# Performance work log

Hardware: AMD Instinct MI355X
Metric: run time of the kernel (lower is better)

## Reference

```python
import jax, jax.numpy as jnp
import numpy as np

B, T, C, HS = 4, 2048, 1024, 64  # batch, seq, n_embd, head_size


def setup_inputs() -> dict:
    key = jax.random.key(0)
    k1, k2, k3, k4 = jax.random.split(key, 4)
    x = jax.random.normal(k1, (B, T, C), dtype=jnp.float32)
    Wq = jax.random.normal(k2, (HS, C), dtype=jnp.float32) * (C ** -0.5)
    Wk = jax.random.normal(k3, (HS, C), dtype=jnp.float32) * (C ** -0.5)
    Wv = jax.random.normal(k4, (HS, C), dtype=jnp.float32) * (C ** -0.5)
    return {"x": x, "Wq": Wq, "Wk": Wk, "Wv": Wv}


def reference(x, Wq, Wk, Wv):
    # q,k,v: [B,T,HS] (nn.Linear: x @ W.T, no bias)
    q = jnp.einsum('btc,hc->bth', x, Wq)
    k = jnp.einsum('btc,hc->bth', x, Wk)
    v = jnp.einsum('btc,hc->bth', x, Wv)
    scale = k.shape[-1] ** -0.5
    wei = jnp.einsum('bth,bsh->bts', q, k) * scale  # [B,T,T]
    # causal mask (tril == 0 -> -inf)
    mask = jnp.tril(jnp.ones((T, T), dtype=bool))
    wei = jnp.where(mask, wei, -jnp.inf)
    wei = jax.nn.softmax(wei, axis=-1)
    # dropout p=0.0 -> identity
    out = jnp.einsum('bts,bsh->bth', wei, v)  # [B,T,HS]
    return out
```

## Files before the change

kernel.cpp:

```cpp
#include <hip/hip_runtime.h>
#include <hip/hip_bf16.h>

#define BB 4
#define TT 2048
#define CC 1024
#define HSZ 64
#define NTOT 8192

typedef __attribute__((ext_vector_type(8))) short bf16x8;
typedef __attribute__((ext_vector_type(4))) float f32x4;

__device__ __forceinline__ unsigned short f2bf(float x) {
    __hip_bfloat16 h = __float2bfloat16(x);
    return *reinterpret_cast<unsigned short*>(&h);
}

__global__ __launch_bounds__(256) void convert_w(
    const float* __restrict__ Wq, const float* __restrict__ Wk,
    const float* __restrict__ Wv, unsigned short* __restrict__ Wh) {
    const int i = blockIdx.x * 256 + threadIdx.x;
    const int c = i >> 8, k4 = (i & 255) * 4;
    float4 wv;
    if (c < 64) {
        wv = *(const float4*)&Wq[(size_t)c * CC + k4];
        wv.x *= 0.125f; wv.y *= 0.125f; wv.z *= 0.125f; wv.w *= 0.125f;
    } else if (c < 128) {
        wv = *(const float4*)&Wk[(size_t)(c - 64) * CC + k4];
    } else {
        wv = *(const float4*)&Wv[(size_t)(c - 128) * CC + k4];
    }
    ushort4 h = {f2bf(wv.x), f2bf(wv.y), f2bf(wv.z), f2bf(wv.w)};
    *(ushort4*)&Wh[(size_t)c * CC + k4] = h;
}

__global__ __launch_bounds__(256) void qkv_mfma(
    const float* __restrict__ x, const unsigned short* __restrict__ Wh,
    unsigned short* __restrict__ qs, unsigned short* __restrict__ ksb,
    unsigned short* __restrict__ vT) {
    __shared__ __align__(16) unsigned short xs[32 * 72];
    __shared__ __align__(16) unsigned short Ws[192 * 72];
    const int tid = threadIdx.x;
    const int w = tid >> 6, lane = tid & 63;
    const int l16 = lane & 15, quad = lane >> 4;
    const int row0 = blockIdx.x * 32;

    const int xrow = tid >> 3, xcol = (tid & 7) * 8;

    float4 xa, xb;
    uint4 wreg0, wreg1, wreg2, wreg3, wreg4, wreg5;

#define LOADX(ch)                                                            \
    {                                                                        \
        const float* p = &x[(size_t)(row0 + xrow) * CC + (ch) * 64 + xcol];  \
        xa = *(const float4*)p;                                              \
        xb = *(const float4*)(p + 4);                                        \
    }
#define LOADW1(it, dst, ch)                                                  \
    {                                                                        \
        const int e = tid + (it) * 256;                                      \
        const int c = e >> 3, g = e & 7;                                     \
        dst = *(const uint4*)&Wh[(size_t)c * CC + (ch) * 64 + g * 8];        \
    }
#define LOADW(ch)                                                            \
    LOADW1(0, wreg0, ch) LOADW1(1, wreg1, ch) LOADW1(2, wreg2, ch)           \
    LOADW1(3, wreg3, ch) LOADW1(4, wreg4, ch) LOADW1(5, wreg5, ch)
#define STOREW1(it, src)                                                     \
    {                                                                        \
        const int e = tid + (it) * 256;                                      \
        const int c = e >> 3, g = e & 7;                                     \
        *(uint4*)&Ws[c * 72 + g * 8] = src;                                  \
    }
#define WRITELDS()                                                           \
    {                                                                        \
        ushort4 h0 = {f2bf(xa.x), f2bf(xa.y), f2bf(xa.z), f2bf(xa.w)};       \
        ushort4 h1 = {f2bf(xb.x), f2bf(xb.y), f2bf(xb.z), f2bf(xb.w)};       \
        *(ushort4*)&xs[xrow * 72 + xcol] = h0;                               \
        *(ushort4*)&xs[xrow * 72 + xcol + 4] = h1;                           \
        STOREW1(0, wreg0) STOREW1(1, wreg1) STOREW1(2, wreg2)                \
        STOREW1(3, wreg3) STOREW1(4, wreg4) STOREW1(5, wreg5)                \
    }

    f32x4 acc[2][3];
#pragma unroll
    for (int m = 0; m < 2; ++m)
#pragma unroll
        for (int n = 0; n < 3; ++n) acc[m][n] = (f32x4){0.f, 0.f, 0.f, 0.f};

    LOADX(0);
    LOADW(0);
    WRITELDS();
    __syncthreads();

    for (int ch = 0; ch < 16; ++ch) {
        if (ch < 15) {
            LOADX(ch + 1);
            LOADW(ch + 1);
        }
        bf16x8 am[2][2], bn[3][2];
#pragma unroll
        for (int m = 0; m < 2; ++m)
#pragma unroll
            for (int h = 0; h < 2; ++h)
                am[m][h] = *(const bf16x8*)&xs[(m * 16 + l16) * 72 + h * 32 + quad * 8];
#pragma unroll
        for (int n = 0; n < 3; ++n)
#pragma unroll
            for (int h = 0; h < 2; ++h)
                bn[n][h] =
                    *(const bf16x8*)&Ws[(w * 48 + n * 16 + l16) * 72 + h * 32 + quad * 8];
#pragma unroll
        for (int h = 0; h < 2; ++h)
#pragma unroll
            for (int m = 0; m < 2; ++m)
#pragma unroll
                for (int n = 0; n < 3; ++n)
                    acc[m][n] = __builtin_amdgcn_mfma_f32_16x16x32_bf16(
                        am[m][h], bn[n][h], acc[m][n], 0, 0, 0);
        if (ch < 15) {
            __syncthreads();
            WRITELDS();
            __syncthreads();
        }
    }

#pragma unroll
    for (int m = 0; m < 2; ++m) {
#pragma unroll
        for (int n = 0; n < 3; ++n) {
            const int col = w * 48 + n * 16 + l16;
            const int r0 = row0 + m * 16 + quad * 4;
            f32x4 a = acc[m][n];
            if (col < 64) {
#pragma unroll
                for (int r = 0; r < 4; ++r)
                    qs[(size_t)(r0 + r) * HSZ + col] = f2bf(a[r]);
            } else if (col < 128) {
#pragma unroll
                for (int r = 0; r < 4; ++r)
                    ksb[(size_t)(r0 + r) * HSZ + (col - 64)] = f2bf(a[r]);
            } else {
                ushort4 pk = {f2bf(a[0]), f2bf(a[1]), f2bf(a[2]), f2bf(a[3])};
                *(ushort4*)&vT[(size_t)(col - 128) * NTOT + r0] = pk;
            }
        }
    }
#undef LOADX
#undef LOADW1
#undef LOADW
#undef STOREW1
#undef WRITELDS
}

__global__ __launch_bounds__(256, 2) void attn_mfma(
    const unsigned short* __restrict__ qs, const unsigned short* __restrict__ ksb,
    const unsigned short* __restrict__ vT, float* __restrict__ out) {
    __shared__ __align__(16) unsigned char smem[17664];
    unsigned short* Ps = (unsigned short*)smem;
    float* Om = (float*)smem;
    float* Lm = (float*)(smem + 17408);

    const int raw = blockIdx.x;
    const int i = (raw < 256) ? raw : 767 - raw;
    const int b = i >> 7;
    const int qt = i & 127;
    const int t0 = qt * 16;
    const int tid = threadIdx.x;
    const int w = tid >> 6, lane = tid & 63;
    const int l16 = lane & 15, quad = lane >> 4;

    const size_t qoff = (size_t)(b * TT + t0 + l16) * HSZ + quad * 8;
    const bf16x8 aq0 = *(const bf16x8*)&qs[qoff];
    const bf16x8 aq1 = *(const bf16x8*)&qs[qoff + 32];

    f32x4 OC[4];
#pragma unroll
    for (int t = 0; t < 4; ++t) OC[t] = (f32x4){0.f, 0.f, 0.f, 0.f};
    float lsum[4] = {0.f, 0.f, 0.f, 0.f};

    const unsigned short* kbase = ksb + (size_t)b * TT * HSZ;
    const int nk = (qt >> 2) + 1;

    for (int j = w; j < nk; j += 4) {
        const int key0 = j * 64;
        bf16x8 cv0[4], cv1[4];
#pragma unroll
        for (int ht = 0; ht < 4; ++ht) {
            const unsigned short* vp =
                vT + (size_t)(ht * 16 + l16) * NTOT + b * TT + key0 + quad * 8;
            cv0[ht] = *(const bf16x8*)vp;
            cv1[ht] = *(const bf16x8*)(vp + 32);
        }
        f32x4 S[4];
#pragma unroll
        for (int nt = 0; nt < 4; ++nt) {
            const unsigned short* kp =
                kbase + (size_t)(key0 + nt * 16 + l16) * HSZ + quad * 8;
            bf16x8 bk0 = *(const bf16x8*)kp;
            bf16x8 bk1 = *(const bf16x8*)(kp + 32);
            f32x4 a = (f32x4){0.f, 0.f, 0.f, 0.f};
            a = __builtin_amdgcn_mfma_f32_16x16x32_bf16(aq0, bk0, a, 0, 0, 0);
            a = __builtin_amdgcn_mfma_f32_16x16x32_bf16(aq1, bk1, a, 0, 0, 0);
            S[nt] = a;
        }
        if (j == nk - 1) {
#pragma unroll
            for (int nt = 0; nt < 4; ++nt) {
                const int key = key0 + nt * 16 + l16;
#pragma unroll
                for (int r = 0; r < 4; ++r)
                    if (key > t0 + quad * 4 + r) S[nt][r] = -1e30f;
            }
        }
#pragma unroll
        for (int nt = 0; nt < 4; ++nt)
#pragma unroll
            for (int r = 0; r < 4; ++r) S[nt][r] = __expf(S[nt][r]);
#pragma unroll
        for (int r = 0; r < 4; ++r)
            lsum[r] += S[0][r] + S[1][r] + S[2][r] + S[3][r];
        unsigned short* Pw = Ps + w * 1152;
#pragma unroll
        for (int nt = 0; nt < 4; ++nt)
#pragma unroll
            for (int r = 0; r < 4; ++r)
                Pw[(quad * 4 + r) * 72 + nt * 16 + l16] = f2bf(S[nt][r]);
        bf16x8 pf0 = *(const bf16x8*)&Pw[l16 * 72 + quad * 8];
        bf16x8 pf1 = *(const bf16x8*)&Pw[l16 * 72 + 32 + quad * 8];
#pragma unroll
        for (int ht = 0; ht < 4; ++ht) {
            f32x4 a = OC[ht];
            a = __builtin_amdgcn_mfma_f32_16x16x32_bf16(pf0, cv0[ht], a, 0, 0, 0);
            a = __builtin_amdgcn_mfma_f32_16x16x32_bf16(pf1, cv1[ht], a, 0, 0, 0);
            OC[ht] = a;
        }
    }
#pragma unroll
    for (int r = 0; r < 4; ++r) {
        float v = lsum[r];
#pragma unroll
        for (int off = 1; off < 16; off <<= 1) v += __shfl_xor(v, off, 64);
        lsum[r] = v;
    }
    __syncthreads();
#pragma unroll
    for (int ht = 0; ht < 4; ++ht)
#pragma unroll
        for (int r = 0; r < 4; ++r)
            Om[(w * 16 + quad * 4 + r) * 68 + ht * 16 + l16] = OC[ht][r];
    if (l16 == 0) {
#pragma unroll
        for (int r = 0; r < 4; ++r) Lm[w * 16 + quad * 4 + r] = lsum[r];
    }
    __syncthreads();
    {
        const int row = tid >> 4, h0 = (tid & 15) * 4;
        float L = 0.f, o0 = 0.f, o1 = 0.f, o2 = 0.f, o3 = 0.f;
#pragma unroll
        for (int w2 = 0; w2 < 4; ++w2) {
            L += Lm[w2 * 16 + row];
            const float* p = &Om[(w2 * 16 + row) * 68 + h0];
            o0 += p[0]; o1 += p[1]; o2 += p[2]; o3 += p[3];
        }
        const float inv = 1.f / L;
        *(float4*)&out[(size_t)(b * TT + t0 + row) * HSZ + h0] =
            (float4){o0 * inv, o1 * inv, o2 * inv, o3 * inv};
    }
}

extern "C" void kernel_launch(void* const* d_in, const int* in_sizes, int n_in,
                              void* d_out, int out_size, void* d_ws, size_t ws_size,
                              hipStream_t stream) {
    const float* x  = (const float*)d_in[0];
    const float* Wq = (const float*)d_in[1];
    const float* Wk = (const float*)d_in[2];
    const float* Wv = (const float*)d_in[3];
    float* out = (float*)d_out;

    unsigned short* qs = (unsigned short*)d_ws;
    unsigned short* ksb = qs + (size_t)NTOT * HSZ;
    unsigned short* vT = ksb + (size_t)NTOT * HSZ;
    unsigned short* Wh = vT + (size_t)NTOT * HSZ;

    convert_w<<<192, 256, 0, stream>>>(Wq, Wk, Wv, Wh);
    qkv_mfma<<<256, 256, 0, stream>>>(x, Wh, qs, ksb, vT);
    attn_mfma<<<512, 256, 0, stream>>>(qs, ksb, vT, out);
}
```

Measured before the change: 108.6 us.

## Fuse weight conversion, QKV projection and attention into one cooperative kernel

Merges the three kernel launches into a single cooperative kernel of 512 blocks, with grid-wide syncs separating weight conversion, QKV projection and causal attention. This removes two kernel launch gaps and the inter-kernel drain/fill bubbles. In exchange it adds two grid barriers, forces a shared 32KB LDS allocation and the stricter 2-blocks-per-CU launch bound on the projection phase, and leaves half the blocks idle during projection.

```diff
diff --git a/kernel.cpp b/kernel.cpp
--- a/kernel.cpp
+++ b/kernel.cpp
@@ -1,5 +1,8 @@
 #include <hip/hip_runtime.h>
 #include <hip/hip_bf16.h>
+#include <hip/hip_cooperative_groups.h>
+
+namespace cg = cooperative_groups;
 
 #define BB 4
 #define TT 2048
@@ -15,39 +18,47 @@
     return *reinterpret_cast<unsigned short*>(&h);
 }
 
-__global__ __launch_bounds__(256) void convert_w(
-    const float* __restrict__ Wq, const float* __restrict__ Wk,
-    const float* __restrict__ Wv, unsigned short* __restrict__ Wh) {
-    const int i = blockIdx.x * 256 + threadIdx.x;
-    const int c = i >> 8, k4 = (i & 255) * 4;
-    float4 wv;
-    if (c < 64) {
-        wv = *(const float4*)&Wq[(size_t)c * CC + k4];
-        wv.x *= 0.125f; wv.y *= 0.125f; wv.z *= 0.125f; wv.w *= 0.125f;
-    } else if (c < 128) {
-        wv = *(const float4*)&Wk[(size_t)(c - 64) * CC + k4];
-    } else {
-        wv = *(const float4*)&Wv[(size_t)(c - 128) * CC + k4];
-    }
-    ushort4 h = {f2bf(wv.x), f2bf(wv.y), f2bf(wv.z), f2bf(wv.w)};
-    *(ushort4*)&Wh[(size_t)c * CC + k4] = h;
-}
-
-__global__ __launch_bounds__(256) void qkv_mfma(
-    const float* __restrict__ x, const unsigned short* __restrict__ Wh,
-    unsigned short* __restrict__ qs, unsigned short* __restrict__ ksb,
-    unsigned short* __restrict__ vT) {
-    __shared__ __align__(16) unsigned short xs[32 * 72];
-    __shared__ __align__(16) unsigned short Ws[192 * 72];
+__global__ __launch_bounds__(256, 2) void fused_head(
+    const float* __restrict__ x, const float* __restrict__ Wq,
+    const float* __restrict__ Wk, const float* __restrict__ Wv,
+    unsigned short* __restrict__ Wh, unsigned short* __restrict__ qs,
+    unsigned short* __restrict__ ksb, unsigned short* __restrict__ vT,
+    float* __restrict__ out) {
+    cg::grid_group grid = cg::this_grid();
+    __shared__ __align__(16) unsigned char smem[32256];
     const int tid = threadIdx.x;
+    const int bid = blockIdx.x;
     const int w = tid >> 6, lane = tid & 63;
     const int l16 = lane & 15, quad = lane >> 4;
-    const int row0 = blockIdx.x * 32;
-
-    const int xrow = tid >> 3, xcol = (tid & 7) * 8;
-
-    float4 xa, xb;
-    uint4 wreg0, wreg1, wreg2, wreg3, wreg4, wreg5;
+
+    {
+        const int i = bid * 256 + tid;
+        if (i < 49152) {
+            const int c = i >> 8, k4 = (i & 255) * 4;
+            float4 wv;
+            if (c < 64) {
+                wv = *(const float4*)&Wq[(size_t)c * CC + k4];
+                wv.x *= 0.125f; wv.y *= 0.125f; wv.z *= 0.125f; wv.w *= 0.125f;
+            } else if (c < 128) {
+                wv = *(const float4*)&Wk[(size_t)(c - 64) * CC + k4];
+            } else {
+                wv = *(const float4*)&Wv[(size_t)(c - 128) * CC + k4];
+            }
+            ushort4 h = {f2bf(wv.x), f2bf(wv.y), f2bf(wv.z), f2bf(wv.w)};
+            *(ushort4*)&Wh[(size_t)c * CC + k4] = h;
+        }
+    }
+    __threadfence();
+    grid.sync();
+
+    if (bid < 256) {
+        unsigned short* xs = (unsigned short*)smem;
+        unsigned short* Ws = (unsigned short*)(smem + 4608);
+        const int row0 = bid * 32;
+        const int xrow = tid >> 3, xcol = (tid & 7) * 8;
+
+        float4 xa, xb;
+        uint4 wreg0, wreg1, wreg2, wreg3, wreg4, wreg5;
 
 #define LOADX(ch)                                                            \
     {                                                                        \
@@ -80,190 +91,188 @@
         STOREW1(3, wreg3) STOREW1(4, wreg4) STOREW1(5, wreg5)                \
     }
 
-    f32x4 acc[2][3];
-#pragma unroll
-    for (int m = 0; m < 2; ++m)
-#pragma unroll
-        for (int n = 0; n < 3; ++n) acc[m][n] = (f32x4){0.f, 0.f, 0.f, 0.f};
-
-    LOADX(0);
-    LOADW(0);
-    WRITELDS();
-    __syncthreads();
-
-    for (int ch = 0; ch < 16; ++ch) {
-        if (ch < 15) {
-            LOADX(ch + 1);
-            LOADW(ch + 1);
-        }
-        bf16x8 am[2][2], bn[3][2];
+        f32x4 acc[2][3];
 #pragma unroll
         for (int m = 0; m < 2; ++m)
 #pragma unroll
+            for (int n = 0; n < 3; ++n) acc[m][n] = (f32x4){0.f, 0.f, 0.f, 0.f};
+
+        LOADX(0);
+        LOADW(0);
+        WRITELDS();
+        __syncthreads();
+
+        for (int ch = 0; ch < 16; ++ch) {
+            if (ch < 15) {
+                LOADX(ch + 1);
+                LOADW(ch + 1);
+            }
+            bf16x8 am[2][2], bn[3][2];
+#pragma unroll
+            for (int m = 0; m < 2; ++m)
+#pragma unroll
+                for (int h = 0; h < 2; ++h)
+                    am[m][h] =
+                        *(const bf16x8*)&xs[(m * 16 + l16) * 72 + h * 32 + quad * 8];
+#pragma unroll
+            for (int n = 0; n < 3; ++n)
+#pragma unroll
+                for (int h = 0; h < 2; ++h)
+                    bn[n][h] = *(const bf16x8*)&Ws[(w * 48 + n * 16 + l16) * 72 +
+                                                   h * 32 + quad * 8];
+#pragma unroll
             for (int h = 0; h < 2; ++h)
-                am[m][h] = *(const bf16x8*)&xs[(m * 16 + l16) * 72 + h * 32 + quad * 8];
-#pragma unroll
-        for (int n = 0; n < 3; ++n)
-#pragma unroll
-            for (int h = 0; h < 2; ++h)
-                bn[n][h] =
-                    *(const bf16x8*)&Ws[(w * 48 + n * 16 + l16) * 72 + h * 32 + quad * 8];
-#pragma unroll
-        for (int h = 0; h < 2; ++h)
-#pragma unroll
-            for (int m = 0; m < 2; ++m)
-#pragma unroll
-                for (int n = 0; n < 3; ++n)
-                    acc[m][n] = __builtin_amdgcn_mfma_f32_16x16x32_bf16(
-                        am[m][h], bn[n][h], acc[m][n], 0, 0, 0);
-        if (ch < 15) {
-            __syncthreads();
-            WRITELDS();
-            __syncthreads();
-        }
-    }
-
-#pragma unroll
-    for (int m = 0; m < 2; ++m) {
-#pragma unroll
-        for (int n = 0; n < 3; ++n) {
-            const int col = w * 48 + n * 16 + l16;
-            const int r0 = row0 + m * 16 + quad * 4;
-            f32x4 a = acc[m][n];
-            if (col < 64) {
-#pragma unroll
-                for (int r = 0; r < 4; ++r)
-                    qs[(size_t)(r0 + r) * HSZ + col] = f2bf(a[r]);
-            } else if (col < 128) {
-#pragma unroll
-                for (int r = 0; r < 4; ++r)
-                    ksb[(size_t)(r0 + r) * HSZ + (col - 64)] = f2bf(a[r]);
-            } else {
-                ushort4 pk = {f2bf(a[0]), f2bf(a[1]), f2bf(a[2]), f2bf(a[3])};
-                *(ushort4*)&vT[(size_t)(col - 128) * NTOT + r0] = pk;
-            }
-        }
-    }
+#pragma unroll
+                for (int m = 0; m < 2; ++m)
+#pragma unroll
+                    for (int n = 0; n < 3; ++n)
+                        acc[m][n] = __builtin_amdgcn_mfma_f32_16x16x32_bf16(
+                            am[m][h], bn[n][h], acc[m][n], 0, 0, 0);
+            if (ch < 15) {
+                __syncthreads();
+                WRITELDS();
+                __syncthreads();
+            }
+        }
+
+#pragma unroll
+        for (int m = 0; m < 2; ++m) {
+#pragma unroll
+            for (int n = 0; n < 3; ++n) {
+                const int col = w * 48 + n * 16 + l16;
+                const int r0 = row0 + m * 16 + quad * 4;
+                f32x4 a = acc[m][n];
+                if (col < 64) {
+#pragma unroll
+                    for (int r = 0; r < 4; ++r)
+                        qs[(size_t)(r0 + r) * HSZ + col] = f2bf(a[r]);
+                } else if (col < 128) {
+#pragma unroll
+                    for (int r = 0; r < 4; ++r)
+                        ksb[(size_t)(r0 + r) * HSZ + (col - 64)] = f2bf(a[r]);
+                } else {
+                    ushort4 pk = {f2bf(a[0]), f2bf(a[1]), f2bf(a[2]), f2bf(a[3])};
+                    *(ushort4*)&vT[(size_t)(col - 128) * NTOT + r0] = pk;
+                }
+            }
+        }
 #undef LOADX
 #undef LOADW1
 #undef LOADW
 #undef STOREW1
 #undef WRITELDS
-}
-
-__global__ __launch_bounds__(256, 2) void attn_mfma(
-    const unsigned short* __restrict__ qs, const unsigned short* __restrict__ ksb,
-    const unsigned short* __restrict__ vT, float* __restrict__ out) {
-    __shared__ __align__(16) unsigned char smem[17664];
-    unsigned short* Ps = (unsigned short*)smem;
-    float* Om = (float*)smem;
-    float* Lm = (float*)(smem + 17408);
-
-    const int raw = blockIdx.x;
-    const int i = (raw < 256) ? raw : 767 - raw;
-    const int b = i >> 7;
-    const int qt = i & 127;
-    const int t0 = qt * 16;
-    const int tid = threadIdx.x;
-    const int w = tid >> 6, lane = tid & 63;
-    const int l16 = lane & 15, quad = lane >> 4;
-
-    const size_t qoff = (size_t)(b * TT + t0 + l16) * HSZ + quad * 8;
-    const bf16x8 aq0 = *(const bf16x8*)&qs[qoff];
-    const bf16x8 aq1 = *(const bf16x8*)&qs[qoff + 32];
-
-    f32x4 OC[4];
-#pragma unroll
-    for (int t = 0; t < 4; ++t) OC[t] = (f32x4){0.f, 0.f, 0.f, 0.f};
-    float lsum[4] = {0.f, 0.f, 0.f, 0.f};
-
-    const unsigned short* kbase = ksb + (size_t)b * TT * HSZ;
-    const int nk = (qt >> 2) + 1;
-
-    for (int j = w; j < nk; j += 4) {
-        const int key0 = j * 64;
-        bf16x8 cv0[4], cv1[4];
-#pragma unroll
-        for (int ht = 0; ht < 4; ++ht) {
-            const unsigned short* vp =
-                vT + (size_t)(ht * 16 + l16) * NTOT + b * TT + key0 + quad * 8;
-            cv0[ht] = *(const bf16x8*)vp;
-            cv1[ht] = *(const bf16x8*)(vp + 32);
-        }
-        f32x4 S[4];
-#pragma unroll
-        for (int nt = 0; nt < 4; ++nt) {
-            const unsigned short* kp =
-                kbase + (size_t)(key0 + nt * 16 + l16) * HSZ + quad * 8;
-            bf16x8 bk0 = *(const bf16x8*)kp;
-            bf16x8 bk1 = *(const bf16x8*)(kp + 32);
-            f32x4 a = (f32x4){0.f, 0.f, 0.f, 0.f};
-            a = __builtin_amdgcn_mfma_f32_16x16x32_bf16(aq0, bk0, a, 0, 0, 0);
-            a = __builtin_amdgcn_mfma_f32_16x16x32_bf16(aq1, bk1, a, 0, 0, 0);
-            S[nt] = a;
-        }
-        if (j == nk - 1) {
+    }
+    __threadfence();
+    grid.sync();
+
+    {
+        unsigned short* Ps = (unsigned short*)smem;
+        float* Om = (float*)smem;
+        float* Lm = (float*)(smem + 17408);
+
+        const int raw = bid;
+        const int i = (raw < 256) ? raw : 767 - raw;
+        const int b = i >> 7;
+        const int qt = i & 127;
+        const int t0 = qt * 16;
+
+        const size_t qoff = (size_t)(b * TT + t0 + l16) * HSZ + quad * 8;
+        const bf16x8 aq0 = *(const bf16x8*)&qs[qoff];
+        const bf16x8 aq1 = *(const bf16x8*)&qs[qoff + 32];
+
+        f32x4 OC[4];
+#pragma unroll
+        for (int t = 0; t < 4; ++t) OC[t] = (f32x4){0.f, 0.f, 0.f, 0.f};
+        float lsum[4] = {0.f, 0.f, 0.f, 0.f};
+
+        const unsigned short* kbase = ksb + (size_t)b * TT * HSZ;
+        const int nk = (qt >> 2) + 1;
+
+        for (int j = w; j < nk; j += 4) {
+            const int key0 = j * 64;
+            bf16x8 cv0[4], cv1[4];
+#pragma unroll
+            for (int ht = 0; ht < 4; ++ht) {
+                const unsigned short* vp =
+                    vT + (size_t)(ht * 16 + l16) * NTOT + b * TT + key0 + quad * 8;
+                cv0[ht] = *(const bf16x8*)vp;
+                cv1[ht] = *(const bf16x8*)(vp + 32);
+            }
+            f32x4 S[4];
 #pragma unroll
             for (int nt = 0; nt < 4; ++nt) {
-                const int key = key0 + nt * 16 + l16;
+                const unsigned short* kp =
+                    kbase + (size_t)(key0 + nt * 16 + l16) * HSZ + quad * 8;
+                bf16x8 bk0 = *(const bf16x8*)kp;
+                bf16x8 bk1 = *(const bf16x8*)(kp + 32);
+                f32x4 a = (f32x4){0.f, 0.f, 0.f, 0.f};
+                a = __builtin_amdgcn_mfma_f32_16x16x32_bf16(aq0, bk0, a, 0, 0, 0);
+                a = __builtin_amdgcn_mfma_f32_16x16x32_bf16(aq1, bk1, a, 0, 0, 0);
+                S[nt] = a;
+            }
+            if (j == nk - 1) {
+#pragma unroll
+                for (int nt = 0; nt < 4; ++nt) {
+                    const int key = key0 + nt * 16 + l16;
+#pragma unroll
+                    for (int r = 0; r < 4; ++r)
+                        if (key > t0 + quad * 4 + r) S[nt][r] = -1e30f;
+                }
+            }
+#pragma unroll
+            for (int nt = 0; nt < 4; ++nt)
+#pragma unroll
+                for (int r = 0; r < 4; ++r) S[nt][r] = __expf(S[nt][r]);
+#pragma unroll
+            for (int r = 0; r < 4; ++r)
+                lsum[r] += S[0][r] + S[1][r] + S[2][r] + S[3][r];
+            unsigned short* Pw = Ps + w * 1152;
+#pragma unroll
+            for (int nt = 0; nt < 4; ++nt)
 #pragma unroll
                 for (int r = 0; r < 4; ++r)
-                    if (key > t0 + quad * 4 + r) S[nt][r] = -1e30f;
-            }
-        }
-#pragma unroll
-        for (int nt = 0; nt < 4; ++nt)
-#pragma unroll
-            for (int r = 0; r < 4; ++r) S[nt][r] = __expf(S[nt][r]);
-#pragma unroll
-        for (int r = 0; r < 4; ++r)
-            lsum[r] += S[0][r] + S[1][r] + S[2][r] + S[3][r];
-        unsigned short* Pw = Ps + w * 1152;
-#pragma unroll
-        for (int nt = 0; nt < 4; ++nt)
+                    Pw[(quad * 4 + r) * 72 + nt * 16 + l16] = f2bf(S[nt][r]);
+            bf16x8 pf0 = *(const bf16x8*)&Pw[l16 * 72 + quad * 8];
+            bf16x8 pf1 = *(const bf16x8*)&Pw[l16 * 72 + 32 + quad * 8];
+#pragma unroll
+            for (int ht = 0; ht < 4; ++ht) {
+                f32x4 a = OC[ht];
+                a = __builtin_amdgcn_mfma_f32_16x16x32_bf16(pf0, cv0[ht], a, 0, 0, 0);
+                a = __builtin_amdgcn_mfma_f32_16x16x32_bf16(pf1, cv1[ht], a, 0, 0, 0);
+                OC[ht] = a;
+            }
+        }
+#pragma unroll
+        for (int r = 0; r < 4; ++r) {
+            float v = lsum[r];
+#pragma unroll
+            for (int off = 1; off < 16; off <<= 1) v += __shfl_xor(v, off, 64);
+            lsum[r] = v;
+        }
+        __syncthreads();
+#pragma unroll
+        for (int ht = 0; ht < 4; ++ht)
 #pragma unroll
             for (int r = 0; r < 4; ++r)
-                Pw[(quad * 4 + r) * 72 + nt * 16 + l16] = f2bf(S[nt][r]);
-        bf16x8 pf0 = *(const bf16x8*)&Pw[l16 * 72 + quad * 8];
-        bf16x8 pf1 = *(const bf16x8*)&Pw[l16 * 72 + 32 + quad * 8];
-#pragma unroll
-        for (int ht = 0; ht < 4; ++ht) {
-            f32x4 a = OC[ht];
-            a = __builtin_amdgcn_mfma_f32_16x16x32_bf16(pf0, cv0[ht], a, 0, 0, 0);
-            a = __builtin_amdgcn_mfma_f32_16x16x32_bf16(pf1, cv1[ht], a, 0, 0, 0);
-            OC[ht] = a;
-        }
-    }
-#pragma unroll
-    for (int r = 0; r < 4; ++r) {
-        float v = lsum[r];
-#pragma unroll
-        for (int off = 1; off < 16; off <<= 1) v += __shfl_xor(v, off, 64);
-        lsum[r] = v;
-    }
-    __syncthreads();
-#pragma unroll
-    for (int ht = 0; ht < 4; ++ht)
-#pragma unroll
-        for (int r = 0; r < 4; ++r)
-            Om[(w * 16 + quad * 4 + r) * 68 + ht * 16 + l16] = OC[ht][r];
-    if (l16 == 0) {
-#pragma unroll
-        for (int r = 0; r < 4; ++r) Lm[w * 16 + quad * 4 + r] = lsum[r];
-    }
-    __syncthreads();
-    {
-        const int row = tid >> 4, h0 = (tid & 15) * 4;
-        float L = 0.f, o0 = 0.f, o1 = 0.f, o2 = 0.f, o3 = 0.f;
-#pragma unroll
-        for (int w2 = 0; w2 < 4; ++w2) {
-            L += Lm[w2 * 16 + row];
-            const float* p = &Om[(w2 * 16 + row) * 68 + h0];
-            o0 += p[0]; o1 += p[1]; o2 += p[2]; o3 += p[3];
-        }
-        const float inv = 1.f / L;
-        *(float4*)&out[(size_t)(b * TT + t0 + row) * HSZ + h0] =
-            (float4){o0 * inv, o1 * inv, o2 * inv, o3 * inv};
+                Om[(w * 16 + quad * 4 + r) * 68 + ht * 16 + l16] = OC[ht][r];
+        if (l16 == 0) {
+#pragma unroll
+            for (int r = 0; r < 4; ++r) Lm[w * 16 + quad * 4 + r] = lsum[r];
+        }
+        __syncthreads();
+        {
+            const int row = tid >> 4, h0 = (tid & 15) * 4;
+            float L = 0.f, o0 = 0.f, o1 = 0.f, o2 = 0.f, o3 = 0.f;
+#pragma unroll
+            for (int w2 = 0; w2 < 4; ++w2) {
+                L += Lm[w2 * 16 + row];
+                const float* p = &Om[(w2 * 16 + row) * 68 + h0];
+                o0 += p[0]; o1 += p[1]; o2 += p[2]; o3 += p[3];
+            }
+            const float inv = 1.f / L;
+            *(float4*)&out[(size_t)(b * TT + t0 + row) * HSZ + h0] =
+                (float4){o0 * inv, o1 * inv, o2 * inv, o3 * inv};
+        }
     }
 }
 
@@ -281,7 +290,8 @@
     unsigned short* vT = ksb + (size_t)NTOT * HSZ;
     unsigned short* Wh = vT + (size_t)NTOT * HSZ;
 
-    convert_w<<<192, 256, 0, stream>>>(Wq, Wk, Wv, Wh);
-    qkv_mfma<<<256, 256, 0, stream>>>(x, Wh, qs, ksb, vT);
-    attn_mfma<<<512, 256, 0, stream>>>(qs, ksb, vT, out);
+    void* args[] = {(void*)&x, (void*)&Wq, (void*)&Wk, (void*)&Wv,
+                    (void*)&Wh, (void*)&qs, (void*)&ksb, (void*)&vT, (void*)&out};
+    hipLaunchCooperativeKernel((const void*)fused_head, dim3(512), dim3(256),
+                               args, 0, stream);
 }
```

Measured after the change: 327.8 us. 3.02x slower.
